# Optimization experiments

Hardware: AMD Instinct MI355X
Metric: run time of the kernel (lower is better)

## Reference

```python
import jax, jax.numpy as jnp
import numpy as np

NHEAD = 16


def corrcoef(X, Y):
    # X, Y: [..., S, D]; Pearson correlation between rows of X and rows of Y
    X = X - X.mean(-1, keepdims=True)
    Y = Y - Y.mean(-1, keepdims=True)
    c = jnp.einsum('...id,...jd->...ij', X, Y)            # [..., S, S]
    d = jnp.einsum('...id,...id->...i', X, Y)             # diagonal of c
    stddev = jnp.sqrt(d)
    c = c / stddev[..., :, None]
    c = c / stddev[..., None, :]
    c = jnp.clip(c, -1.0, 1.0)
    return jnp.where(jnp.isnan(c), 0.0, c)


def setup_inputs() -> dict:
    key = jax.random.key(0)
    k1, k2, k3 = jax.random.split(key, 3)
    T, B, D = 2048, 2, 1024
    query = jax.random.normal(k1, (T, B, D), dtype=jnp.float32)
    W_qkv = jax.random.normal(k2, (3 * D, D), dtype=jnp.float32) * (1.0 / np.sqrt(D))
    b_qkv = jax.random.normal(k3, (3 * D,), dtype=jnp.float32) * 0.01
    return {"query": query, "W_qkv": W_qkv, "b_qkv": b_qkv}


def reference(query, W_qkv, b_qkv):
    T, B, D = query.shape
    hd = D // NHEAD
    qkv = query @ W_qkv.T + b_qkv                          # [T, B, 3D]
    q, k, v = jnp.split(qkv, 3, axis=-1)

    def to_bhsd(x):
        return x.reshape(T, B, NHEAD, hd).transpose(1, 2, 0, 3)  # [B, H, S, hd]

    q, k, v = to_bhsd(q), to_bhsd(k), to_bhsd(v)
    corr = corrcoef(q, k)                                   # [B, H, S, S]
    corr = jax.nn.softmax(corr, axis=-1)                    # eval: dropout_p = 0
    return corr @ v                                         # [B, H, S, hd]
```

## Files before the change

kernel.cpp:

```cpp
#include <hip/hip_runtime.h>

#define S 2048
#define D 1024
#define NH 16
#define HD 64
#define N3 3072
#define M 4096

typedef short s16x8 __attribute__((ext_vector_type(8)));
typedef _Float16 f16x8 __attribute__((ext_vector_type(8)));
typedef float f32x4 __attribute__((ext_vector_type(4)));
typedef unsigned int u32;

__device__ __forceinline__ unsigned short f2bf(float f) {
  unsigned u = __builtin_bit_cast(unsigned, f);
  u += 0x7fffu + ((u >> 16) & 1u);
  return (unsigned short)(u >> 16);
}
__device__ __forceinline__ float bf2f(unsigned short h) {
  return __builtin_bit_cast(float, (unsigned)h << 16);
}

__device__ __forceinline__ float wsum(float v) {
  #pragma unroll
  for (int m = 1; m < 64; m <<= 1) v += __shfl_xor(v, m, 64);
  return v;
}

__device__ __forceinline__ void gload_lds16(const unsigned short* g, unsigned short* l) {
  __builtin_amdgcn_global_load_lds(
      (const __attribute__((address_space(1))) u32*)g,
      (__attribute__((address_space(3))) u32*)l, 16, 0, 0);
}

__global__ __launch_bounds__(256) void split_k(const float* __restrict__ q,
                                               const float* __restrict__ w,
                                               unsigned short* __restrict__ A1,
                                               unsigned short* __restrict__ A2,
                                               unsigned short* __restrict__ W1,
                                               unsigned short* __restrict__ W2) {
  const size_t gid = (size_t)blockIdx.x * 256 + threadIdx.x;
  const size_t NA = (size_t)M * D / 4;
  float4 x;
  unsigned short* p1; unsigned short* p2; size_t qi; float scale;
  if (gid < NA) {
    qi = gid;  x = ((const float4*)q)[qi];
    p1 = A1; p2 = A2; scale = 64.f;
  } else {
    qi = gid - NA;  x = ((const float4*)w)[qi];
    p1 = W1; p2 = W2; scale = 1024.f;
  }
  float e[4] = {x.x * scale, x.y * scale, x.z * scale, x.w * scale};
  unsigned short h1[4], h2[4];
  #pragma unroll
  for (int i = 0; i < 4; ++i) {
    _Float16 a = (_Float16)e[i];
    float r = e[i] - (float)a;
    _Float16 b = (_Float16)r;
    h1[i] = __builtin_bit_cast(unsigned short, a);
    h2[i] = __builtin_bit_cast(unsigned short, b);
  }
  *(ushort4*)&p1[qi * 4] = make_ushort4(h1[0], h1[1], h1[2], h1[3]);
  *(ushort4*)&p2[qi * 4] = make_ushort4(h2[0], h2[1], h2[2], h2[3]);
}

__global__ __launch_bounds__(256) void gemm_mfma(const unsigned short* __restrict__ A1,
                                                 const unsigned short* __restrict__ A2,
                                                 const unsigned short* __restrict__ W1,
                                                 const unsigned short* __restrict__ W2,
                                                 const float* __restrict__ bias,
                                                 float* __restrict__ C) {
  __shared__ unsigned short As[128 * 64];
  __shared__ unsigned short Bs[128 * 64];
  const int tid = threadIdx.x;
  const int w = tid >> 6, l = tid & 63;
  const int lo = l & 15, hi = l >> 4;
  const int n0 = blockIdx.x * 128, m0 = blockIdx.y * 128;
  const int wr = w >> 1, wc = w & 1;

  const int nseg = (n0 >= 2048) ? 1 : 3;

  const int srow = (tid >> 3) & 31;
  const int skc = tid & 7;

  f32x4 acc[4][4];
  #pragma unroll
  for (int mi = 0; mi < 4; ++mi)
    #pragma unroll
    for (int nj = 0; nj < 4; ++nj) acc[mi][nj] = (f32x4){0.f, 0.f, 0.f, 0.f};

  for (int s = 0; s < 3; ++s) {
    if (s >= nseg) break;
    const unsigned short* Ab;
    const unsigned short* Bb;
    switch (s) {
      case 0: Ab = A1; Bb = W1; break;
      case 1: Ab = A2; Bb = W1; break;
      default: Ab = A1; Bb = W2; break;
    }
    Ab += (size_t)m0 * D;
    Bb += (size_t)n0 * D;

    for (int k0 = 0; k0 < D; k0 += 64) {
      __syncthreads();
      #pragma unroll
      for (int c = 0; c < 4; ++c) {
        const int row = c * 32 + srow;
        const int koct = skc ^ (row & 7);
        gload_lds16(Ab + (size_t)row * D + k0 + koct * 8,
                    As + c * 2048 + w * 512);
        gload_lds16(Bb + (size_t)row * D + k0 + koct * 8,
                    Bs + c * 2048 + w * 512);
      }
      __syncthreads();

      f16x8 af[4][2], bf[4][2];
      #pragma unroll
      for (int mi = 0; mi < 4; ++mi)
        #pragma unroll
        for (int ks = 0; ks < 2; ++ks) {
          const int row = wr * 64 + mi * 16 + lo;
          const int koct = (ks * 4 + hi) ^ (lo & 7);
          af[mi][ks] = *(const f16x8*)&As[row * 64 + koct * 8];
        }
      #pragma unroll
      for (int nj = 0; nj < 4; ++nj)
        #pragma unroll
        for (int ks = 0; ks < 2; ++ks) {
          const int row = wc * 64 + nj * 16 + lo;
          const int koct = (ks * 4 + hi) ^ (lo & 7);
          bf[nj][ks] = *(const f16x8*)&Bs[row * 64 + koct * 8];
        }
      #pragma unroll
      for (int mi = 0; mi < 4; ++mi)
        #pragma unroll
        for (int nj = 0; nj < 4; ++nj)
          #pragma unroll
          for (int ks = 0; ks < 2; ++ks)
            acc[mi][nj] = __builtin_amdgcn_mfma_f32_16x16x32_f16(
                af[mi][ks], bf[nj][ks], acc[mi][nj], 0, 0, 0);
    }
  }

  #pragma unroll
  for (int mi = 0; mi < 4; ++mi)
    #pragma unroll
    for (int nj = 0; nj < 4; ++nj) {
      const int n = n0 + wc * 64 + nj * 16 + lo;
      const float bj = bias[n];
      #pragma unroll
      for (int r = 0; r < 4; ++r) {
        const int m = m0 + wr * 64 + mi * 16 + hi * 4 + r;
        C[(size_t)m * N3 + n] = acc[mi][nj][r] * (1.f / 65536.f) + bj;
      }
    }
}

__global__ __launch_bounds__(256) void stats_k(const float* __restrict__ qkv,
                                               unsigned short* __restrict__ qhi,
                                               unsigned short* __restrict__ qlo,
                                               unsigned short* __restrict__ khi,
                                               unsigned short* __restrict__ klo,
                                               unsigned short* __restrict__ vt) {
  __shared__ unsigned short VsT[64][65];
  const int tt = blockIdx.x, bh = blockIdx.y;
  const int b = bh >> 4, h = bh & 15;
  const int w = threadIdx.x >> 6, l = threadIdx.x & 63;

  for (int rr = 0; rr < 16; ++rr) {
    const int t = tt * 64 + w * 16 + rr;
    const size_t base = (size_t)(t * 2 + b) * N3 + h * HD;
    const float q = qkv[base + l];
    const float k = qkv[base + D + l];
    const float v = qkv[base + 2 * D + l];
    const float qm = wsum(q) * (1.f / 64.f);
    const float km = wsum(k) * (1.f / 64.f);
    const float qcv = q - qm, kcv = k - km;
    const float d = wsum(qcv * kcv);
    float rv = 0.f;
    if (d > 0.f) {
      rv = rsqrtf(d);
      rv = rv * (1.5f - 0.5f * d * rv * rv);
    }
    const float qn = qcv * rv, kn = kcv * rv;
    const size_t ro = ((size_t)bh * S + t) * HD + l;
    const unsigned short qh = f2bf(qn);
    const unsigned short kh = f2bf(kn);
    qhi[ro] = qh;  qlo[ro] = f2bf(qn - bf2f(qh));
    khi[ro] = kh;  klo[ro] = f2bf(kn - bf2f(kh));
    VsT[l][w * 16 + rr] = f2bf(v);
  }
  __syncthreads();
  const int dd = threadIdx.x >> 2, seg = threadIdx.x & 3;
  unsigned pk[8];
  #pragma unroll
  for (int e = 0; e < 8; ++e) {
    unsigned l2 = VsT[dd][seg * 16 + 2 * e];
    unsigned h2 = VsT[dd][seg * 16 + 2 * e + 1];
    pk[e] = l2 | (h2 << 16);
  }
  unsigned short* dst = vt + ((size_t)bh * HD + dd) * S + tt * 64 + seg * 16;
  *(uint4*)dst       = make_uint4(pk[0], pk[1], pk[2], pk[3]);
  *(uint4*)(dst + 8) = make_uint4(pk[4], pk[5], pk[6], pk[7]);
}

__global__ __launch_bounds__(512) void attn_k(const unsigned short* __restrict__ qhi,
                                              const unsigned short* __restrict__ qlo,
                                              const unsigned short* __restrict__ khi,
                                              const unsigned short* __restrict__ klo,
                                              const unsigned short* __restrict__ vt,
                                              float* __restrict__ out) {
  __shared__ unsigned short Kh[64 * 64];
  __shared__ unsigned short Kl[64 * 64];
  __shared__ unsigned short Vsm[64 * 64];
  __shared__ unsigned short Ps[128 * 64];

  const int tid = threadIdx.x;
  const int w = tid >> 6, l = tid & 63;
  const int lo = l & 15, hi = l >> 4;

  const int wgid = blockIdx.x;
  const int orig = (wgid & 7) * 64 + (wgid >> 3);
  const int bh = orig >> 4, qt = orig & 15;

  const unsigned short* qhb = qhi + (size_t)bh * S * HD;
  const unsigned short* qlb = qlo + (size_t)bh * S * HD;
  const unsigned short* khb = khi + (size_t)bh * S * HD;
  const unsigned short* klb = klo + (size_t)bh * S * HD;
  const unsigned short* vbase = vt + (size_t)bh * HD * S;
  const int qrow0 = qt * 128 + w * 16;

  const int srow = tid >> 3;
  const int sg = (tid & 7) ^ (srow & 7);

  s16x8 aqh[2], aql[2];
  #pragma unroll
  for (int ks = 0; ks < 2; ++ks) {
    const size_t off = (size_t)(qrow0 + lo) * HD + ks * 32 + hi * 8;
    aqh[ks] = *(const s16x8*)(qhb + off);
    aql[ks] = *(const s16x8*)(qlb + off);
  }

  f32x4 oacc[4];
  float den[4];
  #pragma unroll
  for (int nd = 0; nd < 4; ++nd) { oacc[nd] = (f32x4){0.f, 0.f, 0.f, 0.f}; den[nd] = 0.f; }

  for (int j0 = 0; j0 < S; j0 += 64) {
    __syncthreads();
    {
      const size_t kgo = (size_t)(j0 + srow) * HD + sg * 8;
      gload_lds16(khb + kgo, Kh + w * 512);
      gload_lds16(klb + kgo, Kl + w * 512);
      gload_lds16(vbase + (size_t)srow * S + j0 + sg * 8, Vsm + w * 512);
    }
    __syncthreads();

    #pragma unroll
    for (int nj = 0; nj < 4; ++nj) {
      f32x4 acc = (f32x4){0.f, 0.f, 0.f, 0.f};
      #pragma unroll
      for (int ks = 0; ks < 2; ++ks) {
        const int off = (nj * 16 + lo) * 64 + (((ks * 4 + hi) ^ (lo & 7)) << 3);
        s16x8 bkh = *(const s16x8*)&Kh[off];
        s16x8 bkl = *(const s16x8*)&Kl[off];
        acc = __builtin_amdgcn_mfma_f32_16x16x32_bf16(aqh[ks], bkh, acc, 0, 0, 0);
        acc = __builtin_amdgcn_mfma_f32_16x16x32_bf16(aqh[ks], bkl, acc, 0, 0, 0);
        acc = __builtin_amdgcn_mfma_f32_16x16x32_bf16(aql[ks], bkh, acc, 0, 0, 0);
      }
      #pragma unroll
      for (int r = 0; r < 4; ++r) {
        float c = fminf(1.f, fmaxf(-1.f, acc[r]));
        const float e = __expf(c);
        den[r] += e;
        const int pr = w * 16 + hi * 4 + r;
        Ps[pr * 64 + ((((nj * 2) + (lo >> 3)) ^ (pr & 7)) << 3) + (lo & 7)] = f2bf(e);
      }
    }

    {
      const int prow = w * 16 + lo;
      s16x8 pa0 = *(const s16x8*)&Ps[prow * 64 + ((hi ^ (lo & 7)) << 3)];
      s16x8 pa1 = *(const s16x8*)&Ps[prow * 64 + (((4 + hi) ^ (lo & 7)) << 3)];
      #pragma unroll
      for (int nd = 0; nd < 4; ++nd) {
        const int vrow = nd * 16 + lo;
        s16x8 bv0 = *(const s16x8*)&Vsm[vrow * 64 + ((hi ^ (lo & 7)) << 3)];
        s16x8 bv1 = *(const s16x8*)&Vsm[vrow * 64 + (((4 + hi) ^ (lo & 7)) << 3)];
        oacc[nd] = __builtin_amdgcn_mfma_f32_16x16x32_bf16(pa0, bv0, oacc[nd], 0, 0, 0);
        oacc[nd] = __builtin_amdgcn_mfma_f32_16x16x32_bf16(pa1, bv1, oacc[nd], 0, 0, 0);
      }
    }
  }

  #pragma unroll
  for (int r = 0; r < 4; ++r) {
    float dsum = den[r];
    dsum += __shfl_xor(dsum, 1, 64);
    dsum += __shfl_xor(dsum, 2, 64);
    dsum += __shfl_xor(dsum, 4, 64);
    dsum += __shfl_xor(dsum, 8, 64);
    den[r] = 1.f / dsum;
  }
  #pragma unroll
  for (int nd = 0; nd < 4; ++nd)
    #pragma unroll
    for (int r = 0; r < 4; ++r) {
      const size_t row = (size_t)bh * S + qrow0 + hi * 4 + r;
      out[row * HD + nd * 16 + lo] = oacc[nd][r] * den[r];
    }
}

extern "C" void kernel_launch(void* const* d_in, const int* in_sizes, int n_in,
                              void* d_out, int out_size, void* d_ws, size_t ws_size,
                              hipStream_t stream) {
  const float* query = (const float*)d_in[0];
  const float* W     = (const float*)d_in[1];
  const float* bias  = (const float*)d_in[2];
  float* out = (float*)d_out;
  char* ws = (char*)d_ws;

  float*          qkv = (float*)ws;
  unsigned short* A1 = (unsigned short*)(ws + 50331648);
  unsigned short* A2 = (unsigned short*)(ws + 58720256);
  unsigned short* W1 = (unsigned short*)(ws + 67108864);
  unsigned short* W2 = (unsigned short*)(ws + 73400320);
  unsigned short* qhi = (unsigned short*)(ws + 50331648);
  unsigned short* qlo = (unsigned short*)(ws + 58720256);
  unsigned short* khi = (unsigned short*)(ws + 67108864);
  unsigned short* klo = (unsigned short*)(ws + 75497472);
  unsigned short* vt  = (unsigned short*)(ws + 83886080);

  split_k  <<<dim3(7168), 256, 0, stream>>>(query, W, A1, A2, W1, W2);
  gemm_mfma<<<dim3(24, 32), 256, 0, stream>>>(A1, A2, W1, W2, bias, qkv);
  stats_k  <<<dim3(32, 32), 256, 0, stream>>>(qkv, qhi, qlo, khi, klo, vt);
  attn_k   <<<dim3(512), 512, 0, stream>>>(qhi, qlo, khi, klo, vt, out);
}
```

Before: 177.7 us.

## Keep softmax probabilities in registers via transposed QK^T and lane shuffles, use fp16 PV

The QK^T MFMA operands are swapped so each lane holds scores for one query column. The exp values are packed to fp16 with cvt_pkrtz and redistributed across lanes with shuffles into the A-operand layout for the PV MFMA, which removes the Ps shared-memory round trip. V is now stored as fp16 and the PV product uses f16 MFMA, and launch bounds request 4 blocks per CU. Many shuffles per tile replace the LDS stores and loads, and the row sums are reduced differently at the end.

New measurement: 176.6 us. No clear change (-0.6%).

```diff
diff --git a/kernel.cpp b/kernel.cpp
--- a/kernel.cpp
+++ b/kernel.cpp
@@ -9,8 +9,10 @@
 
 typedef short s16x8 __attribute__((ext_vector_type(8)));
 typedef _Float16 f16x8 __attribute__((ext_vector_type(8)));
+typedef _Float16 f16x2 __attribute__((ext_vector_type(2)));
 typedef float f32x4 __attribute__((ext_vector_type(4)));
 typedef unsigned int u32;
+typedef u32 u32x4 __attribute__((ext_vector_type(4)));
 
 __device__ __forceinline__ unsigned short f2bf(float f) {
   unsigned u = __builtin_bit_cast(unsigned, f);
@@ -19,6 +21,10 @@
 }
 __device__ __forceinline__ float bf2f(unsigned short h) {
   return __builtin_bit_cast(float, (unsigned)h << 16);
+}
+__device__ __forceinline__ unsigned short f2h(float f) {
+  _Float16 h = (_Float16)f;
+  return __builtin_bit_cast(unsigned short, h);
 }
 
 __device__ __forceinline__ float wsum(float v) {
@@ -188,7 +194,7 @@
     const unsigned short kh = f2bf(kn);
     qhi[ro] = qh;  qlo[ro] = f2bf(qn - bf2f(qh));
     khi[ro] = kh;  klo[ro] = f2bf(kn - bf2f(kh));
-    VsT[l][w * 16 + rr] = f2bf(v);
+    VsT[l][w * 16 + rr] = f2h(v);
   }
   __syncthreads();
   const int dd = threadIdx.x >> 2, seg = threadIdx.x & 3;
@@ -204,16 +210,15 @@
   *(uint4*)(dst + 8) = make_uint4(pk[4], pk[5], pk[6], pk[7]);
 }
 
-__global__ __launch_bounds__(512) void attn_k(const unsigned short* __restrict__ qhi,
-                                              const unsigned short* __restrict__ qlo,
-                                              const unsigned short* __restrict__ khi,
-                                              const unsigned short* __restrict__ klo,
-                                              const unsigned short* __restrict__ vt,
-                                              float* __restrict__ out) {
+__global__ __launch_bounds__(512, 4) void attn_k(const unsigned short* __restrict__ qhi,
+                                                 const unsigned short* __restrict__ qlo,
+                                                 const unsigned short* __restrict__ khi,
+                                                 const unsigned short* __restrict__ klo,
+                                                 const unsigned short* __restrict__ vt,
+                                                 float* __restrict__ out) {
   __shared__ unsigned short Kh[64 * 64];
   __shared__ unsigned short Kl[64 * 64];
   __shared__ unsigned short Vsm[64 * 64];
-  __shared__ unsigned short Ps[128 * 64];
 
   const int tid = threadIdx.x;
   const int w = tid >> 6, l = tid & 63;
@@ -242,9 +247,13 @@
   }
 
   f32x4 oacc[4];
-  float den[4];
-  #pragma unroll
-  for (int nd = 0; nd < 4; ++nd) { oacc[nd] = (f32x4){0.f, 0.f, 0.f, 0.f}; den[nd] = 0.f; }
+  float den = 0.f;
+  #pragma unroll
+  for (int nd = 0; nd < 4; ++nd) oacc[nd] = (f32x4){0.f, 0.f, 0.f, 0.f};
+
+  const int sel = hi >> 1;
+  const int srcA = lo + ((hi & 1) << 5);
+  const int srcB = srcA + 16;
 
   for (int j0 = 0; j0 < S; j0 += 64) {
     __syncthreads();
@@ -256,58 +265,72 @@
     }
     __syncthreads();
 
+    u32 pk2[4][2];
     #pragma unroll
     for (int nj = 0; nj < 4; ++nj) {
       f32x4 acc = (f32x4){0.f, 0.f, 0.f, 0.f};
       #pragma unroll
       for (int ks = 0; ks < 2; ++ks) {
         const int off = (nj * 16 + lo) * 64 + (((ks * 4 + hi) ^ (lo & 7)) << 3);
-        s16x8 bkh = *(const s16x8*)&Kh[off];
-        s16x8 bkl = *(const s16x8*)&Kl[off];
-        acc = __builtin_amdgcn_mfma_f32_16x16x32_bf16(aqh[ks], bkh, acc, 0, 0, 0);
-        acc = __builtin_amdgcn_mfma_f32_16x16x32_bf16(aqh[ks], bkl, acc, 0, 0, 0);
-        acc = __builtin_amdgcn_mfma_f32_16x16x32_bf16(aql[ks], bkh, acc, 0, 0, 0);
+        s16x8 akh = *(const s16x8*)&Kh[off];
+        s16x8 akl = *(const s16x8*)&Kl[off];
+        acc = __builtin_amdgcn_mfma_f32_16x16x32_bf16(akh, aqh[ks], acc, 0, 0, 0);
+        acc = __builtin_amdgcn_mfma_f32_16x16x32_bf16(akl, aqh[ks], acc, 0, 0, 0);
+        acc = __builtin_amdgcn_mfma_f32_16x16x32_bf16(akh, aql[ks], acc, 0, 0, 0);
       }
+      float e[4];
       #pragma unroll
       for (int r = 0; r < 4; ++r) {
         float c = fminf(1.f, fmaxf(-1.f, acc[r]));
-        const float e = __expf(c);
-        den[r] += e;
-        const int pr = w * 16 + hi * 4 + r;
-        Ps[pr * 64 + ((((nj * 2) + (lo >> 3)) ^ (pr & 7)) << 3) + (lo & 7)] = f2bf(e);
+        e[r] = __expf(c);
+        den += e[r];
       }
-    }
-
-    {
-      const int prow = w * 16 + lo;
-      s16x8 pa0 = *(const s16x8*)&Ps[prow * 64 + ((hi ^ (lo & 7)) << 3)];
-      s16x8 pa1 = *(const s16x8*)&Ps[prow * 64 + (((4 + hi) ^ (lo & 7)) << 3)];
-      #pragma unroll
-      for (int nd = 0; nd < 4; ++nd) {
-        const int vrow = nd * 16 + lo;
-        s16x8 bv0 = *(const s16x8*)&Vsm[vrow * 64 + ((hi ^ (lo & 7)) << 3)];
-        s16x8 bv1 = *(const s16x8*)&Vsm[vrow * 64 + (((4 + hi) ^ (lo & 7)) << 3)];
-        oacc[nd] = __builtin_amdgcn_mfma_f32_16x16x32_bf16(pa0, bv0, oacc[nd], 0, 0, 0);
-        oacc[nd] = __builtin_amdgcn_mfma_f32_16x16x32_bf16(pa1, bv1, oacc[nd], 0, 0, 0);
-      }
-    }
-  }
-
-  #pragma unroll
-  for (int r = 0; r < 4; ++r) {
-    float dsum = den[r];
-    dsum += __shfl_xor(dsum, 1, 64);
-    dsum += __shfl_xor(dsum, 2, 64);
-    dsum += __shfl_xor(dsum, 4, 64);
-    dsum += __shfl_xor(dsum, 8, 64);
-    den[r] = 1.f / dsum;
-  }
+      pk2[nj][0] = __builtin_bit_cast(u32, __builtin_amdgcn_cvt_pkrtz(e[0], e[1]));
+      pk2[nj][1] = __builtin_bit_cast(u32, __builtin_amdgcn_cvt_pkrtz(e[2], e[3]));
+    }
+
+    f16x8 pa[2];
+    #pragma unroll
+    for (int ks = 0; ks < 2; ++ks) {
+      u32 a0 = __shfl(pk2[2 * ks][0], srcA, 64);
+      u32 b0 = __shfl(pk2[2 * ks + 1][0], srcA, 64);
+      u32 a1 = __shfl(pk2[2 * ks][1], srcA, 64);
+      u32 b1 = __shfl(pk2[2 * ks + 1][1], srcA, 64);
+      u32 a2 = __shfl(pk2[2 * ks][0], srcB, 64);
+      u32 b2 = __shfl(pk2[2 * ks + 1][0], srcB, 64);
+      u32 a3 = __shfl(pk2[2 * ks][1], srcB, 64);
+      u32 b3 = __shfl(pk2[2 * ks + 1][1], srcB, 64);
+      u32x4 u;
+      u[0] = sel ? b0 : a0;
+      u[1] = sel ? b1 : a1;
+      u[2] = sel ? b2 : a2;
+      u[3] = sel ? b3 : a3;
+      pa[ks] = __builtin_bit_cast(f16x8, u);
+    }
+
+    #pragma unroll
+    for (int nd = 0; nd < 4; ++nd) {
+      const int vrow = nd * 16 + lo;
+      f16x8 bv0 = *(const f16x8*)&Vsm[vrow * 64 + ((hi ^ (lo & 7)) << 3)];
+      f16x8 bv1 = *(const f16x8*)&Vsm[vrow * 64 + (((4 + hi) ^ (lo & 7)) << 3)];
+      oacc[nd] = __builtin_amdgcn_mfma_f32_16x16x32_f16(pa[0], bv0, oacc[nd], 0, 0, 0);
+      oacc[nd] = __builtin_amdgcn_mfma_f32_16x16x32_f16(pa[1], bv1, oacc[nd], 0, 0, 0);
+    }
+  }
+
+  float d1 = den + __shfl_xor(den, 16, 64);
+  float dtot = d1 + __shfl_xor(d1, 32, 64);
+  float inv = 1.f / dtot;
+  float dr[4];
+  #pragma unroll
+  for (int r = 0; r < 4; ++r) dr[r] = __shfl(inv, hi * 4 + r, 64);
+
   #pragma unroll
   for (int nd = 0; nd < 4; ++nd)
     #pragma unroll
     for (int r = 0; r < 4; ++r) {
       const size_t row = (size_t)bh * S + qrow0 + hi * 4 + r;
-      out[row * HD + nd * 16 + lo] = oacc[nd][r] * den[r];
+      out[row * HD + nd * 16 + lo] = oacc[nd][r] * dr[r];
     }
 }
 
```
